# Optimization experiments

Measured on AMD Instinct MI355X. Metric: run time of the kernel, lower is better.

## Reference

```python
import jax, jax.numpy as jnp
import numpy as np

SEED_ID = 1234  # seed_id from init, masked to 32 bits


def _synth_R(k_iter, d_out, d_in, dtype):
    # Seeded pseudo-random base weight: randn(d_out, d_in) / sqrt(d_in)
    s = (SEED_ID ^ int(k_iter)) & 0xFFFFFFFF
    R = jax.random.normal(jax.random.key(s), (d_out, d_in), dtype=dtype)
    return R * np.float32(1.0 / np.sqrt(d_in))


def setup_inputs() -> dict:
    key = jax.random.key(0)
    kx, kv, ku = jax.random.split(key, 3)
    B, S, D, RANK = 32, 4096, 512, 64
    x = jax.random.normal(kx, (B, S, D), dtype=jnp.float32)
    alpha = jnp.float32(1.0)
    U = jnp.zeros((D, RANK), dtype=jnp.float32)
    # match torch init: V ~ N(0,1)/sqrt(rank)
    V = jax.random.normal(kv, (RANK, D), dtype=jnp.float32) * np.float32(1.0 / np.sqrt(RANK))
    bias = jnp.zeros((D,), dtype=jnp.float32)
    return {"x": x, "alpha": alpha, "U": U, "V": V, "bias": bias, "k_iter": 2}


def reference(x, alpha, U, V, bias, k_iter):
    d_out = U.shape[0]
    d_in = V.shape[1]
    dtype = x.dtype
    R = _synth_R(k_iter, d_out, d_in, dtype)                      # [d_out, d_in]
    W = alpha.astype(dtype) * R + (U.astype(dtype) @ V.astype(dtype))  # [d_out, d_in]
    # F.linear: x @ W.T + b
    return jnp.einsum('bsd,od->bso', x, W) + bias.astype(dtype)
```

## Files before the change

### kernel.cpp

```cpp
#include <hip/hip_runtime.h>
#include <stdint.h>


#define M_TOTAL 131072
#define N_DIM 512
#define K_DIM 512
#define RANK 64

typedef __attribute__((ext_vector_type(8))) short bf16x8;
typedef __attribute__((ext_vector_type(4))) float f32x4;

__device__ __forceinline__ void threefry2x32(uint32_t k0, uint32_t k1,
                                             uint32_t x0, uint32_t x1,
                                             uint32_t& y0, uint32_t& y1) {
  uint32_t ks2 = k0 ^ k1 ^ 0x1BD11BDAu;
  const uint32_t ks[3] = {k0, k1, ks2};
  const int R0[4] = {13, 15, 26, 6};
  const int R1[4] = {17, 29, 16, 24};
  x0 += ks[0];
  x1 += ks[1];
#pragma unroll
  for (int g = 0; g < 5; ++g) {
    const int* r = (g & 1) ? R1 : R0;
#pragma unroll
    for (int i = 0; i < 4; ++i) {
      x0 += x1;
      x1 = (x1 << r[i]) | (x1 >> (32 - r[i]));
      x1 ^= x0;
    }
    x0 += ks[(g + 1) % 3];
    x1 += ks[(g + 2) % 3] + (uint32_t)(g + 1);
  }
  y0 = x0;
  y1 = x1;
}

__device__ __forceinline__ float erfinv_f32(float x) {
  float w = -log1pf(-x * x);
  float p;
  if (w < 5.0f) {
    w = w - 2.5f;
    p = 2.81022636e-08f;
    p = fmaf(p, w, 3.43273939e-07f);
    p = fmaf(p, w, -3.5233877e-06f);
    p = fmaf(p, w, -4.39150654e-06f);
    p = fmaf(p, w, 0.00021858087f);
    p = fmaf(p, w, -0.00125372503f);
    p = fmaf(p, w, -0.00417768164f);
    p = fmaf(p, w, 0.246640727f);
    p = fmaf(p, w, 1.50140941f);
  } else {
    w = sqrtf(w) - 3.0f;
    p = -0.000200214257f;
    p = fmaf(p, w, 0.000100950558f);
    p = fmaf(p, w, 0.00134934322f);
    p = fmaf(p, w, -0.00367342844f);
    p = fmaf(p, w, 0.00573950773f);
    p = fmaf(p, w, -0.0076224613f);
    p = fmaf(p, w, 0.00943887047f);
    p = fmaf(p, w, 1.00167406f);
    p = fmaf(p, w, 2.83297682f);
  }
  return p * x;
}

__device__ __forceinline__ unsigned short f32_to_bf16_rtne(float f) {
  uint32_t x = __float_as_uint(f);
  uint32_t r = (x + 0x7FFFu + ((x >> 16) & 1u)) >> 16;
  return (unsigned short)r;
}

__global__ __launch_bounds__(256) void build_w_kernel(
    const float* __restrict__ alpha_p, const float* __restrict__ U,
    const float* __restrict__ V, const int* __restrict__ k_iter_p,
    unsigned short* __restrict__ Wb) {
  int idx = blockIdx.x * blockDim.x + threadIdx.x;
  uint32_t s = (1234u ^ (uint32_t)(*k_iter_p));
  uint32_t y0, y1;
  threefry2x32(0u, s, 0u, (uint32_t)idx, y0, y1);
  uint32_t bits = y0 ^ y1;
  float u01 = __uint_as_float((bits >> 9) | 0x3f800000u) - 1.0f;
  const float lo = -0.99999994f;
  float u = fmaxf(lo, u01 * 2.0f + lo);
  float rnorm = 1.41421354f * erfinv_f32(u);
  const float scale = 0.044194173824159216f;

  int o = idx >> 9;
  int i = idx & 511;
  float uv = 0.0f;
#pragma unroll 8
  for (int r = 0; r < RANK; ++r)
    uv = fmaf(U[o * RANK + r], V[r * N_DIM + i], uv);

  float w = (*alpha_p) * (rnorm * scale) + uv;
  Wb[idx] = f32_to_bf16_rtne(w);
}

#define BM 128
#define BN 128
#define BK 64
#define LDK 72
#define NKT (K_DIM / BK)

__global__ __launch_bounds__(256, 3) void gemm_kernel(
    const float* __restrict__ X, const unsigned short* __restrict__ Wb,
    const float* __restrict__ bias, float* __restrict__ Out) {
  __shared__ unsigned short As[BM][LDK];
  __shared__ unsigned short Bs[BN][LDK];

  const int tid = threadIdx.x;
  const int p = blockIdx.x;
  const int l = (p & 7) * 512 + (p >> 3);
  const int nb = l & 3;
  const int mb = l >> 2;
  const int m0 = mb * BM;
  const int n0 = nb * BN;

  const int lane = tid & 63;
  const int wave = tid >> 6;
  const int wr = wave >> 1;
  const int wc = wave & 1;

  f32x4 acc[4][4];
#pragma unroll
  for (int i = 0; i < 4; ++i)
#pragma unroll
    for (int j = 0; j < 4; ++j) acc[i][j] = (f32x4){0.f, 0.f, 0.f, 0.f};

  const int xr = tid >> 4;
  const int xc = (tid & 15) * 4;
  const int wrow = tid >> 3;
  const int wcol = (tid & 7) * 8;

  float4 xv[8];
  bf16x8 wv[4];

#define ISSUE_LOADS(kt_)                                                   \
  {                                                                        \
    const int k0_ = (kt_)*BK;                                              \
    _Pragma("unroll") for (int j = 0; j < 8; ++j) xv[j] =                  \
        *reinterpret_cast<const float4*>(                                  \
            &X[(size_t)(m0 + xr + j * 16) * K_DIM + k0_ + xc]);            \
    _Pragma("unroll") for (int j = 0; j < 4; ++j) wv[j] =                  \
        *reinterpret_cast<const bf16x8*>(                                  \
            &Wb[(size_t)(n0 + wrow + j * 32) * K_DIM + k0_ + wcol]);       \
  }

#define WRITE_LDS()                                                        \
  {                                                                        \
    _Pragma("unroll") for (int j = 0; j < 8; ++j) {                        \
      uint32_t p0_, p1_;                                                   \
      asm("v_cvt_pk_bf16_f32 %0, %1, %2"                                   \
          : "=v"(p0_)                                                      \
          : "v"(xv[j].x), "v"(xv[j].y));                                   \
      asm("v_cvt_pk_bf16_f32 %0, %1, %2"                                   \
          : "=v"(p1_)                                                      \
          : "v"(xv[j].z), "v"(xv[j].w));                                   \
      uint2 pk_;                                                           \
      pk_.x = p0_;                                                         \
      pk_.y = p1_;                                                         \
      *reinterpret_cast<uint2*>(&As[xr + j * 16][xc]) = pk_;               \
    }                                                                      \
    _Pragma("unroll") for (int j = 0; j < 4; ++j)                          \
        *reinterpret_cast<bf16x8*>(&Bs[wrow + j * 32][wcol]) = wv[j];      \
  }

  ISSUE_LOADS(0)
  WRITE_LDS()
  __syncthreads();

  for (int kt = 0; kt < NKT; ++kt) {
    if (kt < NKT - 1) {
      ISSUE_LOADS(kt + 1)
      asm volatile("" ::: "memory");
    }

#pragma unroll
    for (int ks = 0; ks < 2; ++ks) {
      bf16x8 a[4], b[4];
#pragma unroll
      for (int i = 0; i < 4; ++i)
        a[i] = *reinterpret_cast<const bf16x8*>(
            &As[wr * 64 + i * 16 + (lane & 15)][ks * 32 + (lane >> 4) * 8]);
#pragma unroll
      for (int j = 0; j < 4; ++j)
        b[j] = *reinterpret_cast<const bf16x8*>(
            &Bs[wc * 64 + j * 16 + (lane & 15)][ks * 32 + (lane >> 4) * 8]);
#pragma unroll
      for (int i = 0; i < 4; ++i)
#pragma unroll
        for (int j = 0; j < 4; ++j)
          acc[i][j] = __builtin_amdgcn_mfma_f32_16x16x32_bf16(a[i], b[j],
                                                              acc[i][j], 0, 0, 0);
    }
    __syncthreads();

    if (kt < NKT - 1) {
      WRITE_LDS()
      __syncthreads();
    }
  }

  const int col = lane & 15;
  const int rbase = (lane >> 4) * 4;
#pragma unroll
  for (int j = 0; j < 4; ++j) {
    int oc = n0 + wc * 64 + j * 16 + col;
    float bv = bias[oc];
#pragma unroll
    for (int i = 0; i < 4; ++i) {
      int orow = m0 + wr * 64 + i * 16 + rbase;
#pragma unroll
      for (int q = 0; q < 4; ++q) {
        Out[(size_t)(orow + q) * N_DIM + oc] = acc[i][j][q] + bv;
      }
    }
  }
#undef ISSUE_LOADS
#undef WRITE_LDS
}

extern "C" void kernel_launch(void* const* d_in, const int* in_sizes, int n_in,
                              void* d_out, int out_size, void* d_ws,
                              size_t ws_size, hipStream_t stream) {
  (void)in_sizes;
  (void)n_in;
  (void)out_size;
  (void)ws_size;
  const float* x = (const float*)d_in[0];
  const float* alpha = (const float*)d_in[1];
  const float* U = (const float*)d_in[2];
  const float* V = (const float*)d_in[3];
  const float* bias = (const float*)d_in[4];
  const int* k_iter = (const int*)d_in[5];
  float* out = (float*)d_out;
  unsigned short* Wb = (unsigned short*)d_ws;

  build_w_kernel<<<(N_DIM * K_DIM) / 256, 256, 0, stream>>>(alpha, U, V,
                                                            k_iter, Wb);
  const int grid = (M_TOTAL / BM) * (N_DIM / BN);
  gemm_kernel<<<grid, 256, 0, stream>>>(x, Wb, bias, out);
}
```

Measured before the change: 165.0 us.

## Deepen GEMM global-load prefetch to two register stages, relax occupancy bound

The GEMM main loop now double-buffers its register staging for X and W tiles, issuing global loads two K-steps ahead instead of one. The K loop is fully unrolled so the buffer slot indices are compile-time constants. The launch bound drops from 3 to 2 blocks per CU to make room for the extra staging registers. The aim is to hide more global-memory latency in this bandwidth-heavy fp32-input GEMM, at the cost of lower occupancy.

After: 188.9 us. +14.5%, slower.

```diff
diff --git a/kernel.cpp b/kernel.cpp
--- a/kernel.cpp
+++ b/kernel.cpp
@@ -100,9 +100,9 @@
 #define BN 128
 #define BK 64
 #define LDK 72
-#define NKT (K_DIM / BK)
-
-__global__ __launch_bounds__(256, 3) void gemm_kernel(
+#define NSTEP 8
+
+__global__ __launch_bounds__(256, 2) void gemm_kernel(
     const float* __restrict__ X, const unsigned short* __restrict__ Wb,
     const float* __restrict__ bias, float* __restrict__ Out) {
   __shared__ unsigned short As[BM][LDK];
@@ -132,48 +132,47 @@
   const int wrow = tid >> 3;
   const int wcol = (tid & 7) * 8;
 
-  float4 xv[8];
-  bf16x8 wv[4];
-
-#define ISSUE_LOADS(kt_)                                                   \
+  float4 xv[2][8];
+  bf16x8 wv[2][4];
+
+#define ISSUE_LOADS(kt_, s_)                                               \
   {                                                                        \
     const int k0_ = (kt_)*BK;                                              \
-    _Pragma("unroll") for (int j = 0; j < 8; ++j) xv[j] =                  \
+    _Pragma("unroll") for (int j = 0; j < 8; ++j) xv[s_][j] =              \
         *reinterpret_cast<const float4*>(                                  \
             &X[(size_t)(m0 + xr + j * 16) * K_DIM + k0_ + xc]);            \
-    _Pragma("unroll") for (int j = 0; j < 4; ++j) wv[j] =                  \
+    _Pragma("unroll") for (int j = 0; j < 4; ++j) wv[s_][j] =              \
         *reinterpret_cast<const bf16x8*>(                                  \
             &Wb[(size_t)(n0 + wrow + j * 32) * K_DIM + k0_ + wcol]);       \
   }
 
-#define WRITE_LDS()                                                        \
+#define WRITE_LDS(s_)                                                      \
   {                                                                        \
     _Pragma("unroll") for (int j = 0; j < 8; ++j) {                        \
       uint32_t p0_, p1_;                                                   \
       asm("v_cvt_pk_bf16_f32 %0, %1, %2"                                   \
           : "=v"(p0_)                                                      \
-          : "v"(xv[j].x), "v"(xv[j].y));                                   \
+          : "v"(xv[s_][j].x), "v"(xv[s_][j].y));                           \
       asm("v_cvt_pk_bf16_f32 %0, %1, %2"                                   \
           : "=v"(p1_)                                                      \
-          : "v"(xv[j].z), "v"(xv[j].w));                                   \
+          : "v"(xv[s_][j].z), "v"(xv[s_][j].w));                           \
       uint2 pk_;                                                           \
       pk_.x = p0_;                                                         \
       pk_.y = p1_;                                                         \
       *reinterpret_cast<uint2*>(&As[xr + j * 16][xc]) = pk_;               \
     }                                                                      \
     _Pragma("unroll") for (int j = 0; j < 4; ++j)                          \
-        *reinterpret_cast<bf16x8*>(&Bs[wrow + j * 32][wcol]) = wv[j];      \
-  }
-
-  ISSUE_LOADS(0)
-  WRITE_LDS()
+        *reinterpret_cast<bf16x8*>(&Bs[wrow + j * 32][wcol]) = wv[s_][j];  \
+  }
+
+  ISSUE_LOADS(0, 0)
+  ISSUE_LOADS(1, 1)
+  WRITE_LDS(0)
   __syncthreads();
 
-  for (int kt = 0; kt < NKT; ++kt) {
-    if (kt < NKT - 1) {
-      ISSUE_LOADS(kt + 1)
-      asm volatile("" ::: "memory");
-    }
+#pragma unroll
+  for (int kt = 0; kt < NSTEP; ++kt) {
+    if (kt < NSTEP - 2) ISSUE_LOADS(kt + 2, kt & 1)
 
 #pragma unroll
     for (int ks = 0; ks < 2; ++ks) {
@@ -195,8 +194,8 @@
     }
     __syncthreads();
 
-    if (kt < NKT - 1) {
-      WRITE_LDS()
+    if (kt < NSTEP - 1) {
+      WRITE_LDS((kt + 1) & 1)
       __syncthreads();
     }
   }
```
